# Optimization experiments

Measured on AMD Instinct MI355X. Metric: run time of the kernel, lower is better.

## Reference

```python
import jax, jax.numpy as jnp
import numpy as np

N = 500000
D = 256
B = 4096

def setup_inputs() -> dict:
    key = jax.random.key(0)
    k1, k2, k3, k4 = jax.random.split(key, 4)
    x = jax.random.normal(k1, (N, D), dtype=jnp.float32)
    batch = jnp.sort(jax.random.randint(k2, (N,), 0, B))
    w = jax.random.normal(k3, (D,), dtype=jnp.float32) / np.sqrt(D)
    b = jax.random.normal(k4, (), dtype=jnp.float32) * 0.01
    return {"x": x, "w": w, "b": b, "batch": batch, "num_segments": B}

def reference(x, w, b, batch, num_segments):
    # gate_nn: Linear(num_features, 1) -> squeeze(-1)
    scores = x @ w + b                                   # [N]
    # scatter_softmax over segments (numerically stable)
    seg_max = jax.ops.segment_max(scores, batch, num_segments=num_segments)  # [B]
    shifted = scores - seg_max[batch]
    e = jnp.exp(shifted)                                 # [N]
    denom = jax.ops.segment_sum(e, batch, num_segments=num_segments)         # [B]
    attn = e / denom[batch]                              # [N]
    # scatter_sum of attention-weighted features
    out = jax.ops.segment_sum(x * attn[:, None], batch, num_segments=num_segments)  # [B, D]
    return out
```

## Files before the change

### kernel.cpp

```cpp
#include <hip/hip_runtime.h>
#include <math.h>

#define D 256
#define BLOCK 256
#define NWAVES 4
#define R 4

typedef float f32x4 __attribute__((ext_vector_type(4)));

__global__ void seg_bounds_kernel(const int* __restrict__ batch,
                                  int* __restrict__ starts, int N, int B)
{
    int i = blockIdx.x * blockDim.x + threadIdx.x;
    const int stride = gridDim.x * blockDim.x;
    for (; i < N; i += stride) {
        const int cur  = batch[i];
        const int prev = (i == 0) ? -1 : batch[i - 1];
        for (int s = prev + 1; s <= cur; ++s) starts[s] = i;
        if (i == N - 1)
            for (int s = cur + 1; s <= B; ++s) starts[s] = N;
    }
}

__global__ __launch_bounds__(BLOCK, 4) void niche_attn_kernel(
    const float* __restrict__ x,
    const float* __restrict__ w,
    const float* __restrict__ bptr,
    const int*   __restrict__ starts,
    float*       __restrict__ out)
{
    const int seg  = blockIdx.x;
    const int tid  = threadIdx.x;
    const int wave = tid >> 6;
    const int lane = tid & 63;

    __shared__ float s_m[NWAVES];
    __shared__ float s_l[NWAVES];
    __shared__ float s_acc[NWAVES][D];

    const int row_start = starts[seg];
    const int row_end   = starts[seg + 1];

    float* outp = out + (size_t)seg * D;

    if (row_end <= row_start) {
        outp[tid] = 0.f;
        return;
    }

    const int   col  = lane << 2;
    const f32x4 w4   = *(const f32x4*)(w + col);
    const float bias = *bptr;

    float m = -INFINITY;
    float l = 0.f;
    f32x4 acc = {0.f, 0.f, 0.f, 0.f};

    const int step = NWAVES * R;
    int row = row_start + wave * R;

    f32x4 bufA[R], bufB[R];

    auto loadc = [&](f32x4* buf, int r0) {
#pragma unroll
        for (int i = 0; i < R; ++i) {
            int r = r0 + i; r = (r < row_end) ? r : (row_end - 1);
            buf[i] = __builtin_nontemporal_load(
                         (const f32x4*)(x + (size_t)r * D + col));
        }
    };

    auto compute = [&](const f32x4* buf, int r0) {
        float s[R];
#pragma unroll
        for (int i = 0; i < R; ++i)
            s[i] = buf[i].x * w4.x + buf[i].y * w4.y
                 + buf[i].z * w4.z + buf[i].w * w4.w;
#pragma unroll
        for (int off = 32; off > 0; off >>= 1) {
#pragma unroll
            for (int i = 0; i < R; ++i)
                s[i] += __shfl_xor(s[i], off, 64);
        }
#pragma unroll
        for (int i = 0; i < R; ++i)
            s[i] = (r0 + i < row_end) ? (s[i] + bias) : -INFINITY;

        const float cmax = fmaxf(fmaxf(s[0], s[1]), fmaxf(s[2], s[3]));
        const float newm = fmaxf(m, cmax);
        const float alpha = __expf(m - newm);
        float p[R];
#pragma unroll
        for (int i = 0; i < R; ++i)
            p[i] = __expf(s[i] - newm);

        l = l * alpha + ((p[0] + p[1]) + (p[2] + p[3]));
        acc.x *= alpha; acc.y *= alpha; acc.z *= alpha; acc.w *= alpha;
#pragma unroll
        for (int i = 0; i < R; ++i) {
            acc.x = fmaf(buf[i].x, p[i], acc.x);
            acc.y = fmaf(buf[i].y, p[i], acc.y);
            acc.z = fmaf(buf[i].z, p[i], acc.z);
            acc.w = fmaf(buf[i].w, p[i], acc.w);
        }
        m = newm;
    };

    if (row < row_end) loadc(bufA, row);
    while (row < row_end) {
        int nrow = row + step;
        loadc(bufB, nrow);
        compute(bufA, row);
        row = nrow;
        if (row >= row_end) break;
        nrow = row + step;
        loadc(bufA, nrow);
        compute(bufB, row);
        row = nrow;
    }

    if (lane == 0) { s_m[wave] = m; s_l[wave] = l; }
    __syncthreads();

    const float M = fmaxf(fmaxf(s_m[0], s_m[1]), fmaxf(s_m[2], s_m[3]));
    float L = 0.f;
#pragma unroll
    for (int wv = 0; wv < NWAVES; ++wv)
        L += s_l[wv] * __expf(s_m[wv] - M);

    const float scale = __expf(m - M);
    s_acc[wave][col + 0] = acc.x * scale;
    s_acc[wave][col + 1] = acc.y * scale;
    s_acc[wave][col + 2] = acc.z * scale;
    s_acc[wave][col + 3] = acc.w * scale;
    __syncthreads();

    const float invL = 1.f / L;
    const float v = (s_acc[0][tid] + s_acc[1][tid]) + (s_acc[2][tid] + s_acc[3][tid]);
    outp[tid] = v * invL;
}

extern "C" void kernel_launch(void* const* d_in, const int* in_sizes, int n_in,
                              void* d_out, int out_size, void* d_ws, size_t ws_size,
                              hipStream_t stream)
{
    const float* x     = (const float*)d_in[0];
    const float* w     = (const float*)d_in[1];
    const float* b     = (const float*)d_in[2];
    const int*   batch = (const int*)d_in[3];
    float*       out   = (float*)d_out;
    int*         starts = (int*)d_ws;

    const int N = in_sizes[3];
    const int B = out_size / D;

    seg_bounds_kernel<<<1024, BLOCK, 0, stream>>>(batch, starts, N, B);
    niche_attn_kernel<<<B, BLOCK, 0, stream>>>(x, w, b, starts, out);
}
```

Baseline: 622.7 us.

## Map one wave per segment with triple-buffered chunk loads and no LDS reduction

Changes the work split so each 64-lane wave handles a whole segment instead of four waves sharing one. This removes the shared-memory combine and both block barriers. The main loop now prefetches in full 4-row chunks with three register buffers, plus a separate remainder pass, and uses regular loads instead of nontemporal ones. In exchange each segment (~122 rows) is streamed by a single wave, so per-wave memory parallelism depends on the deeper prefetch and on having more concurrent waves.

```diff
diff --git a/kernel.cpp b/kernel.cpp
--- a/kernel.cpp
+++ b/kernel.cpp
@@ -3,7 +3,7 @@
 
 #define D 256
 #define BLOCK 256
-#define NWAVES 4
+#define WPB 4
 #define R 4
 
 typedef float f32x4 __attribute__((ext_vector_type(4)));
@@ -27,55 +27,53 @@
     const float* __restrict__ w,
     const float* __restrict__ bptr,
     const int*   __restrict__ starts,
-    float*       __restrict__ out)
+    float*       __restrict__ out, int B)
 {
-    const int seg  = blockIdx.x;
-    const int tid  = threadIdx.x;
-    const int wave = tid >> 6;
-    const int lane = tid & 63;
+    int seg = blockIdx.x * WPB + (threadIdx.x >> 6);
+    seg = __builtin_amdgcn_readfirstlane(seg);
+    if (seg >= B) return;
 
-    __shared__ float s_m[NWAVES];
-    __shared__ float s_l[NWAVES];
-    __shared__ float s_acc[NWAVES][D];
+    const int lane = threadIdx.x & 63;
+    const int col  = lane << 2;
 
     const int row_start = starts[seg];
     const int row_end   = starts[seg + 1];
-
     float* outp = out + (size_t)seg * D;
 
     if (row_end <= row_start) {
-        outp[tid] = 0.f;
+        f32x4 z = {0.f, 0.f, 0.f, 0.f};
+        *(f32x4*)(outp + col) = z;
         return;
     }
 
-    const int   col  = lane << 2;
     const f32x4 w4   = *(const f32x4*)(w + col);
     const float bias = *bptr;
 
-    float m = -INFINITY;
-    float l = 0.f;
+    float m = -INFINITY, l = 0.f;
     f32x4 acc = {0.f, 0.f, 0.f, 0.f};
 
-    const int step = NWAVES * R;
-    int row = row_start + wave * R;
+    const int len   = row_end - row_start;
+    const int nfull = len >> 2;
+    const int rem   = len & 3;
 
-    f32x4 bufA[R], bufB[R];
+    const float* sbase = x + (size_t)row_start * D;
 
-    auto loadc = [&](f32x4* buf, int r0) {
+    auto loadchunk = [&](f32x4* buf, int t) {
+        const float* p = sbase + (size_t)t * (R * D) + col;
+#pragma unroll
+        for (int i = 0; i < R; ++i)
+            buf[i] = *(const f32x4*)(p + i * D);
+    };
+
+    auto computec = [&](const f32x4* buf, int valid) {
+        float s[R];
 #pragma unroll
         for (int i = 0; i < R; ++i) {
-            int r = r0 + i; r = (r < row_end) ? r : (row_end - 1);
-            buf[i] = __builtin_nontemporal_load(
-                         (const f32x4*)(x + (size_t)r * D + col));
+            float t0 = buf[i].x * w4.x;
+            t0   = fmaf(buf[i].y, w4.y, t0);
+            t0   = fmaf(buf[i].z, w4.z, t0);
+            s[i] = fmaf(buf[i].w, w4.w, t0);
         }
-    };
-
-    auto compute = [&](const f32x4* buf, int r0) {
-        float s[R];
-#pragma unroll
-        for (int i = 0; i < R; ++i)
-            s[i] = buf[i].x * w4.x + buf[i].y * w4.y
-                 + buf[i].z * w4.z + buf[i].w * w4.w;
 #pragma unroll
         for (int off = 32; off > 0; off >>= 1) {
 #pragma unroll
@@ -84,7 +82,7 @@
         }
 #pragma unroll
         for (int i = 0; i < R; ++i)
-            s[i] = (r0 + i < row_end) ? (s[i] + bias) : -INFINITY;
+            s[i] = (i < valid) ? (s[i] + bias) : -INFINITY;
 
         const float cmax = fmaxf(fmaxf(s[0], s[1]), fmaxf(s[2], s[3]));
         const float newm = fmaxf(m, cmax);
@@ -93,7 +91,6 @@
 #pragma unroll
         for (int i = 0; i < R; ++i)
             p[i] = __expf(s[i] - newm);
-
         l = l * alpha + ((p[0] + p[1]) + (p[2] + p[3]));
         acc.x *= alpha; acc.y *= alpha; acc.z *= alpha; acc.w *= alpha;
 #pragma unroll
@@ -106,54 +103,62 @@
         m = newm;
     };
 
-    if (row < row_end) loadc(bufA, row);
-    while (row < row_end) {
-        int nrow = row + step;
-        loadc(bufB, nrow);
-        compute(bufA, row);
-        row = nrow;
-        if (row >= row_end) break;
-        nrow = row + step;
-        loadc(bufA, nrow);
-        compute(bufB, row);
-        row = nrow;
+    f32x4 bufA[R], bufB[R], bufC[R];
+
+    if (nfull > 0) {
+        const int c1 = (1 < nfull) ? 1 : nfull - 1;
+        const int c2 = (2 < nfull) ? 2 : nfull - 1;
+        loadchunk(bufA, 0);
+        loadchunk(bufB, c1);
+        loadchunk(bufC, c2);
+        int t = 0;
+        for (;;) {
+            computec(bufA, R);
+            if (++t == nfull) break;
+            { int tp = t + 2; tp = (tp < nfull) ? tp : (nfull - 1); loadchunk(bufA, tp); }
+            computec(bufB, R);
+            if (++t == nfull) break;
+            { int tp = t + 2; tp = (tp < nfull) ? tp : (nfull - 1); loadchunk(bufB, tp); }
+            computec(bufC, R);
+            if (++t == nfull) break;
+            { int tp = t + 2; tp = (tp < nfull) ? tp : (nfull - 1); loadchunk(bufC, tp); }
+        }
     }
 
-    if (lane == 0) { s_m[wave] = m; s_l[wave] = l; }
-    __syncthreads();
+    if (rem) {
+        f32x4 tb[R];
+        const int base_r = nfull * R;
+        const int last   = len - 1;
+#pragma unroll
+        for (int i = 0; i < R; ++i) {
+            int r = base_r + i; r = (r <= last) ? r : last;
+            tb[i] = *(const f32x4*)(sbase + (size_t)r * D + col);
+        }
+        computec(tb, rem);
+    }
 
-    const float M = fmaxf(fmaxf(s_m[0], s_m[1]), fmaxf(s_m[2], s_m[3]));
-    float L = 0.f;
-#pragma unroll
-    for (int wv = 0; wv < NWAVES; ++wv)
-        L += s_l[wv] * __expf(s_m[wv] - M);
-
-    const float scale = __expf(m - M);
-    s_acc[wave][col + 0] = acc.x * scale;
-    s_acc[wave][col + 1] = acc.y * scale;
-    s_acc[wave][col + 2] = acc.z * scale;
-    s_acc[wave][col + 3] = acc.w * scale;
-    __syncthreads();
-
-    const float invL = 1.f / L;
-    const float v = (s_acc[0][tid] + s_acc[1][tid]) + (s_acc[2][tid] + s_acc[3][tid]);
-    outp[tid] = v * invL;
+    const float invL = 1.f / l;
+    f32x4 o;
+    o.x = acc.x * invL; o.y = acc.y * invL;
+    o.z = acc.z * invL; o.w = acc.w * invL;
+    *(f32x4*)(outp + col) = o;
 }
 
 extern "C" void kernel_launch(void* const* d_in, const int* in_sizes, int n_in,
                               void* d_out, int out_size, void* d_ws, size_t ws_size,
                               hipStream_t stream)
 {
-    const float* x     = (const float*)d_in[0];
-    const float* w     = (const float*)d_in[1];
-    const float* b     = (const float*)d_in[2];
-    const int*   batch = (const int*)d_in[3];
-    float*       out   = (float*)d_out;
+    const float* x      = (const float*)d_in[0];
+    const float* w      = (const float*)d_in[1];
+    const float* b      = (const float*)d_in[2];
+    const int*   batch  = (const int*)d_in[3];
+    float*       out    = (float*)d_out;
     int*         starts = (int*)d_ws;
 
     const int N = in_sizes[3];
     const int B = out_size / D;
 
     seg_bounds_kernel<<<1024, BLOCK, 0, stream>>>(batch, starts, N, B);
-    niche_attn_kernel<<<B, BLOCK, 0, stream>>>(x, w, b, starts, out);
+    niche_attn_kernel<<<(B + WPB - 1) / WPB, BLOCK, 0, stream>>>(
+        x, w, b, starts, out, B);
 }
```

Result: slower. 665.3 us (+6.8%).
